# Kernel tuning notes

Hardware: AMD Instinct MI355X
Metric: run time of the kernel (lower is better)

The kernel has to match this reference:

```python
import jax, jax.numpy as jnp
import numpy as np

SAMPLE_RATE = 44100.0
MIN_GAIN, MAX_GAIN = -12.0, 12.0
MIN_Q, MAX_Q = 0.1, 10.0
# (min, max) for the 15 normalized control params, in channel order
PARAM_RANGES = np.array([
    (MIN_GAIN, MAX_GAIN), (20.0, 2000.0), (MIN_Q, MAX_Q),      # low shelf
    (MIN_GAIN, MAX_GAIN), (20.0, 200.0), (MIN_Q, MAX_Q),       # band0 peaking
    (MIN_GAIN, MAX_GAIN), (200.0, 2000.0), (MIN_Q, MAX_Q),     # band1 peaking
    (MIN_GAIN, MAX_GAIN), (2000.0, 12000.0), (MIN_Q, MAX_Q),   # band2 peaking
    (MIN_GAIN, MAX_GAIN), (4000.0, 16000.0), (MIN_Q, MAX_Q),   # high shelf
], dtype=np.float32)


def _biquad(gain_db, f0, q, ftype):
    """RBJ cookbook biquad. Inputs shape (bs,), returns (bs, 6) normalized so a0==1."""
    A = 10.0 ** (gain_db / 40.0)
    w0 = 2.0 * jnp.pi * (f0 / SAMPLE_RATE)
    alpha = jnp.sin(w0) / (2.0 * q)
    cw = jnp.cos(w0)
    sA = jnp.sqrt(A)
    if ftype == 'peaking':
        b0 = 1.0 + alpha * A; b1 = -2.0 * cw; b2 = 1.0 - alpha * A
        a0 = 1.0 + alpha / A; a1 = -2.0 * cw; a2 = 1.0 - alpha / A
    elif ftype == 'low_shelf':
        b0 = A * ((A + 1) - (A - 1) * cw + 2 * sA * alpha)
        b1 = 2 * A * ((A - 1) - (A + 1) * cw)
        b2 = A * ((A + 1) - (A - 1) * cw - 2 * sA * alpha)
        a0 = (A + 1) + (A - 1) * cw + 2 * sA * alpha
        a1 = -2 * ((A - 1) + (A + 1) * cw)
        a2 = (A + 1) + (A - 1) * cw - 2 * sA * alpha
    else:  # high_shelf
        b0 = A * ((A + 1) + (A - 1) * cw + 2 * sA * alpha)
        b1 = -2 * A * ((A - 1) + (A + 1) * cw)
        b2 = A * ((A + 1) + (A - 1) * cw - 2 * sA * alpha)
        a0 = (A + 1) - (A - 1) * cw + 2 * sA * alpha
        a1 = 2 * ((A - 1) - (A + 1) * cw)
        a2 = (A + 1) - (A - 1) * cw - 2 * sA * alpha
    coeffs = jnp.stack([b0, b1, b2, a0, a1, a2], axis=-1)
    return coeffs / a0[..., None]


def _compute_sos(p):
    """p: (bs, 15) denormalized params -> sos (bs, 5, 6)."""
    secs = [
        _biquad(p[:, 0], p[:, 1], p[:, 2], 'low_shelf'),
        _biquad(p[:, 3], p[:, 4], p[:, 5], 'peaking'),
        _biquad(p[:, 6], p[:, 7], p[:, 8], 'peaking'),
        _biquad(p[:, 9], p[:, 10], p[:, 11], 'peaking'),
        _biquad(p[:, 12], p[:, 13], p[:, 14], 'high_shelf'),
    ]
    return jnp.stack(secs, axis=1)


def _sosfilt(sos, x):
    """Cascaded 5-section biquad, direct form II transposed, zero initial state.
    sos: (bs, 5, 6), x: (bs, T) -> (bs, T)."""
    b0, b1, b2 = sos[..., 0], sos[..., 1], sos[..., 2]  # each (bs, 5)
    a1, a2 = sos[..., 4], sos[..., 5]

    def step(carry, xt):
        z1, z2 = carry  # (bs, 5) each
        s = xt  # (bs,)
        z1n, z2n = [], []
        for k in range(5):  # fixed small cascade
            y = b0[:, k] * s + z1[:, k]
            z1n.append(b1[:, k] * s - a1[:, k] * y + z2[:, k])
            z2n.append(b2[:, k] * s - a2[:, k] * y)
            s = y
        return (jnp.stack(z1n, 1), jnp.stack(z2n, 1)), s

    bs = x.shape[0]
    z0 = jnp.zeros((bs, 5), x.dtype)
    _, y = jax.lax.scan(step, (z0, z0), x.T)
    return y.T


def setup_inputs() -> dict:
    key = jax.random.key(0)
    k1, k2 = jax.random.split(key)
    x = jax.random.normal(k1, (32, 1, 131072), dtype=jnp.float32)
    control_params = jax.random.uniform(k2, (32, 15, 1), dtype=jnp.float32)
    return {"x": x, "control_params": control_params}


def reference(x, control_params):
    # denormalize: min + p * (max - min)
    lo = jnp.asarray(PARAM_RANGES[:, 0])
    hi = jnp.asarray(PARAM_RANGES[:, 1])
    p = control_params[:, :, 0]  # (bs, 15)
    p_denorm = lo[None, :] + p * (hi - lo)[None, :]
    sos = _compute_sos(p_denorm)           # (bs, 5, 6)
    y = _sosfilt(sos, x[:, 0, :])          # (bs, T)
    return y[:, None, :], sos
```

## Files before the change

kernel.cpp:

```cpp
#include <hip/hip_runtime.h>
#include <math.h>


#define NB 32
#define LCH 16
#define T_LEN 131072
#define CPB 256
#define BPB 32
#define CCH 8192
#define WPB 128
#define NPOW 13

__constant__ double c_lo[15] = {-12.0,   20.0, 0.1,
                                -12.0,   20.0, 0.1,
                                -12.0,  200.0, 0.1,
                                -12.0, 2000.0, 0.1,
                                -12.0, 4000.0, 0.1};
__constant__ double c_hi[15] = { 12.0,  2000.0, 10.0,
                                 12.0,   200.0, 10.0,
                                 12.0,  2000.0, 10.0,
                                 12.0, 12000.0, 10.0,
                                 12.0, 16000.0, 10.0};

__global__ __launch_bounds__(128)
void eq_setup(const float* __restrict__ cp, float* __restrict__ sos_out,
              float* __restrict__ powers)
{
    int b = blockIdx.x;
    int t = threadIdx.x;
    __shared__ float  sc[5][5];
    __shared__ double Abuf[2][10][10];

    if (t < 5) {
        int k = t;
        double p[3];
#pragma unroll
        for (int j = 0; j < 3; ++j) {
            int i = k * 3 + j;
            double pv = (double)cp[b * 15 + i];
            p[j] = c_lo[i] + pv * (c_hi[i] - c_lo[i]);
        }
        double A     = exp(p[0] * (M_LN10 / 40.0));
        double w0    = 2.0 * M_PI * p[1] / 44100.0;
        double alpha = sin(w0) / (2.0 * p[2]);
        double cw    = cos(w0);
        double sA    = sqrt(A);
        double b0, b1, b2, a0, a1, a2;
        if (k == 0) {
            b0 =     A * ((A + 1) - (A - 1) * cw + 2 * sA * alpha);
            b1 = 2 * A * ((A - 1) - (A + 1) * cw);
            b2 =     A * ((A + 1) - (A - 1) * cw - 2 * sA * alpha);
            a0 =          (A + 1) + (A - 1) * cw + 2 * sA * alpha;
            a1 =    -2 * ((A - 1) + (A + 1) * cw);
            a2 =          (A + 1) + (A - 1) * cw - 2 * sA * alpha;
        } else if (k == 4) {
            b0 =     A * ((A + 1) + (A - 1) * cw + 2 * sA * alpha);
            b1 = -2 * A * ((A - 1) + (A + 1) * cw);
            b2 =     A * ((A + 1) + (A - 1) * cw - 2 * sA * alpha);
            a0 =          (A + 1) - (A - 1) * cw + 2 * sA * alpha;
            a1 =     2 * ((A - 1) - (A + 1) * cw);
            a2 =          (A + 1) - (A - 1) * cw - 2 * sA * alpha;
        } else {
            b0 = 1.0 + alpha * A;
            b1 = -2.0 * cw;
            b2 = 1.0 - alpha * A;
            a0 = 1.0 + alpha / A;
            a1 = -2.0 * cw;
            a2 = 1.0 - alpha / A;
        }
        double inv = 1.0 / a0;
        float fb0 = (float)(b0 * inv), fb1 = (float)(b1 * inv), fb2 = (float)(b2 * inv);
        float fa1 = (float)(a1 * inv), fa2 = (float)(a2 * inv);
        float* o = sos_out + (size_t)(b * 5 + k) * 6;
        o[0] = fb0; o[1] = fb1; o[2] = fb2; o[3] = 1.0f; o[4] = fa1; o[5] = fa2;
        sc[k][0] = fb0; sc[k][1] = fb1; sc[k][2] = fb2; sc[k][3] = fa1; sc[k][4] = fa2;
    }
    __syncthreads();

    if (t < 10) {
        double z[10];
#pragma unroll
        for (int i = 0; i < 10; ++i) z[i] = 0.0;
        z[t] = 1.0;
        double s = 0.0;
        double zn[10];
#pragma unroll
        for (int k = 0; k < 5; ++k) {
            double b0 = sc[k][0], b1 = sc[k][1], b2 = sc[k][2];
            double a1 = sc[k][3], a2 = sc[k][4];
            double y = b0 * s + z[2 * k];
            zn[2 * k]     = b1 * s - a1 * y + z[2 * k + 1];
            zn[2 * k + 1] = b2 * s - a2 * y;
            s = y;
        }
#pragma unroll
        for (int r = 0; r < 10; ++r) Abuf[0][r][t] = zn[r];
    }
    __syncthreads();

    int r = t / 10, cc = t % 10;
    int cur = 0;
    for (int sq = 0; sq < 16; ++sq) {
        double acc = 0.0;
        if (t < 100) {
#pragma unroll
            for (int j = 0; j < 10; ++j) acc += Abuf[cur][r][j] * Abuf[cur][j][cc];
        }
        __syncthreads();
        if (t < 100) Abuf[cur ^ 1][r][cc] = acc;
        __syncthreads();
        cur ^= 1;
        if (sq >= 3 && t < 100) {
            int m = sq - 3;
            powers[((size_t)b * NPOW + m) * 100 + t] = (float)Abuf[cur][r][cc];
        }
    }
}

template<bool ACC>
__device__ __forceinline__ void affineT(const float* __restrict__ P,
                                        const float u[10], float v[10])
{
#pragma unroll
    for (int rr = 0; rr < 10; ++rr) {
        const float* rp = P + rr * 10;
        float a = ACC ? v[rr] : 0.0f;
#pragma unroll
        for (int c = 0; c <= (rr | 1); ++c) a = fmaf(rp[c], u[c], a);
        v[rr] = a;
    }
}

__device__ __forceinline__ void matvecT(const float* __restrict__ P, float v[10])
{
    float u[10];
#pragma unroll
    for (int i = 0; i < 10; ++i) u[i] = v[i];
    affineT<false>(P, u, v);
}

__global__ __launch_bounds__(256, 2)
void eq_pass1(const float* __restrict__ x, const float* __restrict__ sos,
              const float* __restrict__ powers, float* __restrict__ es_g,
              float* __restrict__ wt)
{
    int blk = blockIdx.x;
    int b = blk >> 5, sp = blk & (BPB - 1);
    int tid = threadIdx.x;
    int w = tid >> 6, lw = tid & 63;

    const float* s5 = sos + (size_t)(b * 5) * 6;
    float cb0[5], cb1[5], cb2[5], ca1[5], ca2[5];
#pragma unroll
    for (int k = 0; k < 5; ++k) {
        cb0[k] = s5[k * 6 + 0]; cb1[k] = s5[k * 6 + 1]; cb2[k] = s5[k * 6 + 2];
        ca1[k] = s5[k * 6 + 4]; ca2[k] = s5[k * 6 + 5];
    }

    int c = sp * CPB + tid;
    const float* xp = x + (size_t)b * T_LEN + (size_t)c * LCH;
    float xr[LCH];
#pragma unroll
    for (int t0 = 0; t0 < LCH; t0 += 4) {
        float4 xv = *reinterpret_cast<const float4*>(xp + t0);
        xr[t0] = xv.x; xr[t0 + 1] = xv.y; xr[t0 + 2] = xv.z; xr[t0 + 3] = xv.w;
    }

    float z1[5] = {0, 0, 0, 0, 0}, z2[5] = {0, 0, 0, 0, 0};
#pragma unroll
    for (int j = 0; j < LCH; ++j) {
        float s = xr[j];
#pragma unroll
        for (int k = 0; k < 5; ++k) {
            float yk = fmaf(cb0[k], s, z1[k]);
            float u  = fmaf(cb1[k], s, z2[k]);
            z1[k] = fmaf(-ca1[k], yk, u);
            z2[k] = fmaf(-ca2[k], yk, cb2[k] * s);
            s = yk;
        }
    }
    float sv[10];
#pragma unroll
    for (int k = 0; k < 5; ++k) { sv[2 * k] = z1[k]; sv[2 * k + 1] = z2[k]; }

    const float* Pb = powers + (size_t)b * NPOW * 100;
#pragma unroll
    for (int j = 0; j < 6; ++j) {
        const float* P = Pb + j * 100;
        float u[10];
#pragma unroll
        for (int i = 0; i < 10; ++i) u[i] = __shfl_up(sv[i], 1 << j);
        if (lw >= (1 << j)) affineT<true>(P, u, sv);
    }

    float es[10];
#pragma unroll
    for (int i = 0; i < 10; ++i) es[i] = __shfl_up(sv[i], 1);
    if (lw == 0) {
#pragma unroll
        for (int i = 0; i < 10; ++i) es[i] = 0.0f;
    }
    float* ep = es_g + (size_t)b * 10 * CCH + c;
#pragma unroll
    for (int i = 0; i < 10; ++i) ep[(size_t)i * CCH] = es[i];

    if (lw == 63) {
        int wid = sp * 4 + w;
        float* wp = wt + (size_t)(b * WPB + wid) * 10;
#pragma unroll
        for (int i = 0; i < 10; ++i) wp[i] = sv[i];
    }
}

__global__ __launch_bounds__(256, 2)
void eq_pass2(const float* __restrict__ x, const float* __restrict__ sos,
              const float* __restrict__ powers, const float* __restrict__ wt,
              const float* __restrict__ es_g, float* __restrict__ y)
{
    int blk = blockIdx.x;
    int b = blk >> 5, sp = blk & (BPB - 1);
    int tid = threadIdx.x;
    int w = tid >> 6, lw = tid & 63;

    __shared__ float ys[CPB * 17];

    const float* Pb = powers + (size_t)b * NPOW * 100;
    int wid = sp * 4 + w;

    const float* wp = wt + (size_t)(b * WPB + 2 * lw) * 10;
    float t0[10], t1[10];
#pragma unroll
    for (int i = 0; i < 10; ++i) { t0[i] = wp[i]; t1[i] = wp[10 + i]; }

    float tau[10];
#pragma unroll
    for (int i = 0; i < 10; ++i) tau[i] = t1[i];
    affineT<true>(Pb + 6 * 100, t0, tau);

#pragma unroll
    for (int j = 0; j < 6; ++j) {
        const float* P = Pb + (7 + j) * 100;
        float u[10];
#pragma unroll
        for (int i = 0; i < 10; ++i) u[i] = __shfl_up(tau[i], 1 << j);
        if (lw >= (1 << j)) affineT<true>(P, u, tau);
    }

    float e[10];
#pragma unroll
    for (int i = 0; i < 10; ++i) e[i] = __shfl_up(tau[i], 1);
    if (lw == 0) {
#pragma unroll
        for (int i = 0; i < 10; ++i) e[i] = 0.0f;
    }
    float s1[10];
#pragma unroll
    for (int i = 0; i < 10; ++i) s1[i] = t0[i];
    affineT<true>(Pb + 6 * 100, e, s1);

    float F[10];
#pragma unroll
    for (int i = 0; i < 10; ++i)
        F[i] = __shfl((wid & 1) ? s1[i] : e[i], wid >> 1);

    int c = sp * CPB + tid;
    const float* xp = x + (size_t)b * T_LEN + (size_t)c * LCH;
    float xr[LCH];
#pragma unroll
    for (int t2 = 0; t2 < LCH; t2 += 4) {
        float4 xv = *reinterpret_cast<const float4*>(xp + t2);
        xr[t2] = xv.x; xr[t2 + 1] = xv.y; xr[t2 + 2] = xv.z; xr[t2 + 3] = xv.w;
    }

#pragma unroll
    for (int m = 0; m < 6; ++m) {
        if ((lw >> m) & 1) matvecT(Pb + m * 100, F);
    }

    const float* s5 = sos + (size_t)(b * 5) * 6;
    float cb0[5], cb1[5], cb2[5], ca1[5], ca2[5];
#pragma unroll
    for (int k = 0; k < 5; ++k) {
        cb0[k] = s5[k * 6 + 0]; cb1[k] = s5[k * 6 + 1]; cb2[k] = s5[k * 6 + 2];
        ca1[k] = s5[k * 6 + 4]; ca2[k] = s5[k * 6 + 5];
    }

    const float* ep = es_g + (size_t)b * 10 * CCH + c;
    float z1[5], z2[5];
#pragma unroll
    for (int k = 0; k < 5; ++k) {
        z1[k] = F[2 * k]     + ep[(size_t)(2 * k) * CCH];
        z2[k] = F[2 * k + 1] + ep[(size_t)(2 * k + 1) * CCH];
    }

    float* yl = ys + tid * 17;
#pragma unroll
    for (int j = 0; j < LCH; ++j) {
        float s = xr[j];
#pragma unroll
        for (int k = 0; k < 5; ++k) {
            float yk = fmaf(cb0[k], s, z1[k]);
            float u  = fmaf(cb1[k], s, z2[k]);
            z1[k] = fmaf(-ca1[k], yk, u);
            z2[k] = fmaf(-ca2[k], yk, cb2[k] * s);
            s = yk;
        }
        yl[j] = s;
    }
    __syncthreads();

    float* yg = y + (size_t)b * T_LEN + (size_t)sp * (CPB * LCH);
#pragma unroll
    for (int it = 0; it < (CPB * LCH) / (256 * 4); ++it) {
        int i = (tid + it * 256) * 4;
        int p = (i >> 4) * 17 + (i & 15);
        *reinterpret_cast<float4*>(yg + i) =
            make_float4(ys[p], ys[p + 1], ys[p + 2], ys[p + 3]);
    }
}

extern "C" void kernel_launch(void* const* d_in, const int* in_sizes, int n_in,
                              void* d_out, int out_size, void* d_ws, size_t ws_size,
                              hipStream_t stream)
{
    const float* x  = (const float*)d_in[0];
    const float* cp = (const float*)d_in[1];
    float* out = (float*)d_out;
    float* sos = out + (size_t)NB * T_LEN;

    float* powers = (float*)d_ws;
    float* wt     = powers + (size_t)NB * NPOW * 100;
    float* es_g   = wt + (size_t)NB * WPB * 10;

    eq_setup<<<dim3(NB), dim3(128), 0, stream>>>(cp, sos, powers);
    eq_pass1<<<dim3(NB * BPB), dim3(256), 0, stream>>>(x, sos, powers, es_g, wt);
    eq_pass2<<<dim3(NB * BPB), dim3(256), 0, stream>>>(x, sos, powers, wt, es_g, out);
}
```

Measured before the change: 45.05 us.

## Double per-thread chunk length, simplify warp-prefix scan and store outputs directly

Raises the per-thread chunk from 16 to 32 samples, which halves the block count and the number of wavefront carry totals. The cross-wave scan now covers 64 wave totals in one 64-lane pass, so the extra pairing step and its additional matrix applications go away. Pass2 drops the LDS staging buffer and barrier and writes float4 outputs directly from each thread, at the cost of a strided, less coalesced global store pattern. The longer serial recurrence per thread also cuts parallelism and adds register pressure.

Result: faster. 43.67 us (-3.1%).

```diff
diff --git a/kernel.cpp b/kernel.cpp
--- a/kernel.cpp
+++ b/kernel.cpp
@@ -3,13 +3,13 @@
 
 
 #define NB 32
-#define LCH 16
+#define LCH 32
 #define T_LEN 131072
 #define CPB 256
-#define BPB 32
-#define CCH 8192
-#define WPB 128
-#define NPOW 13
+#define BPB 16
+#define CCH 4096
+#define WPB 64
+#define NPOW 12
 
 __constant__ double c_lo[15] = {-12.0,   20.0, 0.1,
                                 -12.0,   20.0, 0.1,
@@ -110,8 +110,8 @@
         if (t < 100) Abuf[cur ^ 1][r][cc] = acc;
         __syncthreads();
         cur ^= 1;
-        if (sq >= 3 && t < 100) {
-            int m = sq - 3;
+        if (sq >= 4 && t < 100) {
+            int m = sq - 4;
             powers[((size_t)b * NPOW + m) * 100 + t] = (float)Abuf[cur][r][cc];
         }
     }
@@ -145,7 +145,7 @@
               float* __restrict__ wt)
 {
     int blk = blockIdx.x;
-    int b = blk >> 5, sp = blk & (BPB - 1);
+    int b = blk >> 4, sp = blk & (BPB - 1);
     int tid = threadIdx.x;
     int w = tid >> 6, lw = tid & 63;
 
@@ -218,50 +218,33 @@
               const float* __restrict__ es_g, float* __restrict__ y)
 {
     int blk = blockIdx.x;
-    int b = blk >> 5, sp = blk & (BPB - 1);
+    int b = blk >> 4, sp = blk & (BPB - 1);
     int tid = threadIdx.x;
     int w = tid >> 6, lw = tid & 63;
 
-    __shared__ float ys[CPB * 17];
-
     const float* Pb = powers + (size_t)b * NPOW * 100;
     int wid = sp * 4 + w;
 
-    const float* wp = wt + (size_t)(b * WPB + 2 * lw) * 10;
-    float t0[10], t1[10];
-#pragma unroll
-    for (int i = 0; i < 10; ++i) { t0[i] = wp[i]; t1[i] = wp[10 + i]; }
-
+    const float* wp = wt + (size_t)(b * WPB + lw) * 10;
     float tau[10];
 #pragma unroll
-    for (int i = 0; i < 10; ++i) tau[i] = t1[i];
-    affineT<true>(Pb + 6 * 100, t0, tau);
+    for (int i = 0; i < 10; ++i) tau[i] = wp[i];
 
 #pragma unroll
     for (int j = 0; j < 6; ++j) {
-        const float* P = Pb + (7 + j) * 100;
+        const float* P = Pb + (6 + j) * 100;
         float u[10];
 #pragma unroll
         for (int i = 0; i < 10; ++i) u[i] = __shfl_up(tau[i], 1 << j);
         if (lw >= (1 << j)) affineT<true>(P, u, tau);
     }
 
-    float e[10];
-#pragma unroll
-    for (int i = 0; i < 10; ++i) e[i] = __shfl_up(tau[i], 1);
-    if (lw == 0) {
-#pragma unroll
-        for (int i = 0; i < 10; ++i) e[i] = 0.0f;
-    }
-    float s1[10];
-#pragma unroll
-    for (int i = 0; i < 10; ++i) s1[i] = t0[i];
-    affineT<true>(Pb + 6 * 100, e, s1);
-
     float F[10];
 #pragma unroll
-    for (int i = 0; i < 10; ++i)
-        F[i] = __shfl((wid & 1) ? s1[i] : e[i], wid >> 1);
+    for (int i = 0; i < 10; ++i) {
+        float iv = __shfl(tau[i], (wid - 1) & 63);
+        F[i] = (wid == 0) ? 0.0f : iv;
+    }
 
     int c = sp * CPB + tid;
     const float* xp = x + (size_t)b * T_LEN + (size_t)c * LCH;
@@ -293,29 +276,24 @@
         z2[k] = F[2 * k + 1] + ep[(size_t)(2 * k + 1) * CCH];
     }
 
-    float* yl = ys + tid * 17;
-#pragma unroll
-    for (int j = 0; j < LCH; ++j) {
-        float s = xr[j];
-#pragma unroll
-        for (int k = 0; k < 5; ++k) {
-            float yk = fmaf(cb0[k], s, z1[k]);
-            float u  = fmaf(cb1[k], s, z2[k]);
-            z1[k] = fmaf(-ca1[k], yk, u);
-            z2[k] = fmaf(-ca2[k], yk, cb2[k] * s);
-            s = yk;
-        }
-        yl[j] = s;
-    }
-    __syncthreads();
-
-    float* yg = y + (size_t)b * T_LEN + (size_t)sp * (CPB * LCH);
-#pragma unroll
-    for (int it = 0; it < (CPB * LCH) / (256 * 4); ++it) {
-        int i = (tid + it * 256) * 4;
-        int p = (i >> 4) * 17 + (i & 15);
-        *reinterpret_cast<float4*>(yg + i) =
-            make_float4(ys[p], ys[p + 1], ys[p + 2], ys[p + 3]);
+    float* yp = y + (size_t)b * T_LEN + (size_t)c * LCH;
+#pragma unroll
+    for (int t0 = 0; t0 < LCH; t0 += 4) {
+        float o4[4];
+#pragma unroll
+        for (int j = 0; j < 4; ++j) {
+            float s = xr[t0 + j];
+#pragma unroll
+            for (int k = 0; k < 5; ++k) {
+                float yk = fmaf(cb0[k], s, z1[k]);
+                float u  = fmaf(cb1[k], s, z2[k]);
+                z1[k] = fmaf(-ca1[k], yk, u);
+                z2[k] = fmaf(-ca2[k], yk, cb2[k] * s);
+                s = yk;
+            }
+            o4[j] = s;
+        }
+        *reinterpret_cast<float4*>(yp + t0) = make_float4(o4[0], o4[1], o4[2], o4[3]);
     }
 }
 
```
